# Performance work log

Measured on AMD Instinct MI355X. Metric: run time of the kernel, lower is better.

The kernel has to match this reference:

```python
import jax, jax.numpy as jnp
import numpy as np

DIM = 1024
NUM_HEADS = 16
HEAD_DIM = DIM // NUM_HEADS
ROPE_THETA = 10000.0
SCALE = HEAD_DIM ** -0.5


def _apply_rope(x, cos, sin):
    # x: [B, H, S, head_dim]; cos/sin: [S, head_dim//2] (broadcast over B, H)
    x_even = x[..., 0::2]
    x_odd = x[..., 1::2]
    rot_even = x_even * cos - x_odd * sin
    rot_odd = x_even * sin + x_odd * cos
    # interleave back: stack on last axis then flatten, matching torch .stack(-1).flatten(-2)
    return jnp.stack([rot_even, rot_odd], axis=-1).reshape(x.shape)


def setup_inputs() -> dict:
    key = jax.random.key(0)
    k0, k1, k2 = jax.random.split(key, 3)
    B, S = 2, 2048
    x = jax.random.normal(k0, (B, S, DIM), dtype=jnp.float32)
    # small_init: std = sqrt(2 / (5*dim))
    qkv_w = jax.random.normal(k1, (3 * DIM, DIM), dtype=jnp.float32) * (2.0 / (5 * DIM)) ** 0.5
    qkv_b = jnp.zeros((3 * DIM,), dtype=jnp.float32)
    # wang_init: std = 2 / num_blocks / sqrt(dim) scaled
    out_w = jax.random.normal(k2, (DIM, DIM), dtype=jnp.float32) * (2.0 / DIM) ** 0.5 / 2.0
    out_b = jnp.zeros((DIM,), dtype=jnp.float32)
    return {"x": x, "qkv_w": qkv_w, "qkv_b": qkv_b, "out_w": out_w, "out_b": out_b, "window_size": 512}


def reference(x, qkv_w, qkv_b, out_w, out_b, window_size):
    B, S, D = x.shape
    qkv = x @ qkv_w.T + qkv_b                          # [B, S, 3D]
    qkv = qkv.reshape(B, S, 3, NUM_HEADS, HEAD_DIM).transpose(2, 0, 3, 1, 4)
    q, k, v = qkv[0], qkv[1], qkv[2]                   # each [B, H, S, hd]

    pos = jnp.arange(S, dtype=jnp.float32)
    inv_freq = 1.0 / (ROPE_THETA ** (jnp.arange(0, HEAD_DIM, 2, dtype=jnp.float32) / HEAD_DIM))
    freqs = pos[:, None] * inv_freq                    # [S, hd//2]
    cos, sin = jnp.cos(freqs), jnp.sin(freqs)
    q = _apply_rope(q, cos, sin)
    k = _apply_rope(k, cos, sin)

    scores = jnp.einsum('bhqd,bhkd->bhqk', q, k) * SCALE
    i = jnp.arange(S)
    mask = (i[:, None] >= i[None, :]) & ((i[:, None] - i[None, :]) < window_size)  # causal sliding window
    scores = jnp.where(mask, scores, -jnp.inf)
    attn = jax.nn.softmax(scores, axis=-1)
    out = jnp.einsum('bhqk,bhkd->bhqd', attn, v)       # [B, H, S, hd]
    out = out.transpose(0, 2, 1, 3).reshape(B, S, D)
    return out @ out_w.T + out_b
```

## Files before the change

### kernel.cpp

```cpp
#include <hip/hip_runtime.h>
#include <hip/hip_bf16.h>
#include <cstdint>
#include <cstddef>

using bf16x8 = __attribute__((ext_vector_type(8))) short;
using f32x4  = __attribute__((ext_vector_type(4))) float;

#define MFMA16(a, b, c) __builtin_amdgcn_mfma_f32_16x16x32_bf16((a), (b), (c), 0, 0, 0)

__device__ __forceinline__ unsigned short f2bf(float f) {
    unsigned int u = __float_as_uint(f);
    u += 0x7fffu + ((u >> 16) & 1u);
    return (unsigned short)(u >> 16);
}
__device__ __forceinline__ uint32_t pack2bf(float a, float b) {
    __hip_bfloat162 h = __float22bfloat162_rn(float2{a, b});
    return *(uint32_t*)&h;
}
__device__ __forceinline__ float bf2f(short x) {
    return __uint_as_float(((uint32_t)(unsigned short)x) << 16);
}

__device__ __forceinline__ void gload_lds16(const void* g, void* l) {
    __builtin_amdgcn_global_load_lds(
        (const __attribute__((address_space(1))) void*)g,
        (__attribute__((address_space(3))) void*)l, 16, 0, 0);
}

#define S_LEN 2048
#define NHEAD 16
#define HDIM  64
#define DIM   1024
#define WIN   512
#define MROWS 4096

__global__ void prep(float* __restrict__ cosT, float* __restrict__ sinT,
                     const float* __restrict__ x, unsigned short* __restrict__ xb,
                     const float* __restrict__ qw, unsigned short* __restrict__ qwb,
                     const float* __restrict__ ow, unsigned short* __restrict__ owb) {
    int t = blockIdx.x * 256 + threadIdx.x;
    if (t < 65536) {
        int s = t >> 5, f = t & 31;
        float invf = powf(10000.0f, -(float)f / 32.0f);
        float ang = (float)s * invf;
        cosT[t] = cosf(ang);
        sinT[t] = sinf(ang);
        return;
    }
    int u = t - 65536;
    const float* src;
    unsigned short* dst;
    int i;
    if (u < 1048576)        { src = x;  dst = xb;  i = u * 4; }
    else if (u < 1835008)   { src = qw; dst = qwb; i = (u - 1048576) * 4; }
    else                    { src = ow; dst = owb; i = (u - 1835008) * 4; }
    float4 v = *(const float4*)(src + i);
    ushort4 o;
    o.x = f2bf(v.x); o.y = f2bf(v.y); o.z = f2bf(v.z); o.w = f2bf(v.w);
    *(ushort4*)(dst + i) = o;
}

__global__ __launch_bounds__(256) void gemm_qkv_fused(
        const unsigned short* __restrict__ A,
        const unsigned short* __restrict__ Bw,
        const float* __restrict__ bias,
        const float* __restrict__ cosT, const float* __restrict__ sinT,
        unsigned short* __restrict__ qbuf,
        unsigned short* __restrict__ kbuf,
        unsigned short* __restrict__ vtb) {
    __shared__ __align__(16) char smem_raw[34816];
    const int tid = threadIdx.x;
    const int lane = tid & 63, w = tid >> 6;
    const int wr = w >> 1, wc = w & 1, lm = lane & 15, lg = lane >> 4;
    const int bx = blockIdx.x, by = blockIdx.y;
    const int row0 = by * 128, col0 = bx * 128;
    const int plane = bx >> 3;
    const int h0 = (bx & 7) * 2;
    const int b = by >> 4, s_base = (by & 15) * 128;

    f32x4 acc[4][4];
#pragma unroll
    for (int m = 0; m < 4; ++m)
#pragma unroll
        for (int n = 0; n < 4; ++n) acc[m][n] = (f32x4){0.f, 0.f, 0.f, 0.f};

    short* As = (short*)smem_raw;
    short* Bs = (short*)(smem_raw + 16384);

    for (int kt = 0; kt < 16; ++kt) {
#pragma unroll
        for (int i = 0; i < 4; ++i) {
            int c = tid + 256 * i;
            int r = c >> 3, gs = (c & 7) ^ (r & 7);
            gload_lds16((const char*)A  + (size_t)(row0 + r) * 2048 + (size_t)kt * 128 + gs * 16, As + c * 8);
            gload_lds16((const char*)Bw + (size_t)(col0 + r) * 2048 + (size_t)kt * 128 + gs * 16, Bs + c * 8);
        }
        __syncthreads();
        bf16x8 af0[4], af1[4], bf0[4], bf1[4];
#pragma unroll
        for (int m = 0; m < 4; ++m) {
            int rl = wr * 64 + m * 16 + lm, rb = rl & 7;
            af0[m] = *(const bf16x8*)&As[rl * 64 + ((lg ^ rb) << 3)];
            af1[m] = *(const bf16x8*)&As[rl * 64 + (((lg + 4) ^ rb) << 3)];
        }
#pragma unroll
        for (int n = 0; n < 4; ++n) {
            int rl = wc * 64 + n * 16 + lm, rb = rl & 7;
            bf0[n] = *(const bf16x8*)&Bs[rl * 64 + ((lg ^ rb) << 3)];
            bf1[n] = *(const bf16x8*)&Bs[rl * 64 + (((lg + 4) ^ rb) << 3)];
        }
#pragma unroll
        for (int m = 0; m < 4; ++m)
#pragma unroll
            for (int n = 0; n < 4; ++n) {
                acc[m][n] = MFMA16(af0[m], bf0[n], acc[m][n]);
                acc[m][n] = MFMA16(af1[m], bf1[n], acc[m][n]);
            }
        __syncthreads();
    }

    unsigned short (*tile)[136] = (unsigned short(*)[136])smem_raw;
    const int lane8 = tid & 7, idx = tid >> 3;

    if (plane < 2) {
#pragma unroll
        for (int m = 0; m < 4; ++m)
#pragma unroll
            for (int n = 0; n < 4; ++n) {
                int colL = wc * 64 + n * 16 + lm;
                float bv = bias[col0 + colL];
#pragma unroll
                for (int r = 0; r < 4; ++r)
                    tile[wr * 64 + m * 16 + lg * 4 + r][colL] = f2bf(acc[m][n][r] + bv);
            }
    } else {
#pragma unroll
        for (int m = 0; m < 4; ++m)
#pragma unroll
            for (int n = 0; n < 4; ++n) {
                int colL = wc * 64 + n * 16 + lm;
                float bv = bias[col0 + colL];
                uint2 pk;
                pk.x = pack2bf(acc[m][n][0] + bv, acc[m][n][1] + bv);
                pk.y = pack2bf(acc[m][n][2] + bv, acc[m][n][3] + bv);
                *(uint2*)&tile[colL][wr * 64 + m * 16 + lg * 4] = pk;
            }
    }
    __syncthreads();

    if (plane < 2) {
        unsigned short* dstp = (plane == 0) ? qbuf : kbuf;
        const float qsc = (plane == 0) ? 0.125f : 1.0f;
        int d0 = lane8 * 8;
#pragma unroll
        for (int j = 0; j < 4; ++j) {
            int srow = idx + 32 * j;
            int s = s_base + srow;
            float4 c4 = *(const float4*)&cosT[s * 32 + (d0 >> 1)];
            float4 s4 = *(const float4*)&sinT[s * 32 + (d0 >> 1)];
#pragma unroll
            for (int hh = 0; hh < 2; ++hh) {
                bf16x8 v = *(const bf16x8*)&tile[srow][hh * 64 + d0];
                float e0 = bf2f(v[0]), o0 = bf2f(v[1]);
                float e1 = bf2f(v[2]), o1 = bf2f(v[3]);
                float e2 = bf2f(v[4]), o2 = bf2f(v[5]);
                float e3 = bf2f(v[6]), o3 = bf2f(v[7]);
                uint4 pk;
                pk.x = pack2bf((e0 * c4.x - o0 * s4.x) * qsc, (e0 * s4.x + o0 * c4.x) * qsc);
                pk.y = pack2bf((e1 * c4.y - o1 * s4.y) * qsc, (e1 * s4.y + o1 * c4.y) * qsc);
                pk.z = pack2bf((e2 * c4.z - o2 * s4.z) * qsc, (e2 * s4.z + o2 * c4.z) * qsc);
                pk.w = pack2bf((e3 * c4.w - o3 * s4.w) * qsc, (e3 * s4.w + o3 * c4.w) * qsc);
                int h = h0 + hh;
                *(uint4*)&dstp[(((size_t)(b * NHEAD + h)) * S_LEN + s) * 64 + d0] = pk;
            }
        }
    } else {
#pragma unroll
        for (int rr = 0; rr < 4; ++rr) {
            int hd = rr * 32 + idx;
            int hh = hd >> 6, d = hd & 63, h = h0 + hh;
#pragma unroll
            for (int j = 0; j < 2; ++j) {
                int s0 = lane8 * 8 + j * 64;
                bf16x8 v = *(const bf16x8*)&tile[hd][s0];
                *(bf16x8*)&vtb[((size_t)(b * NHEAD + h) * 64 + d) * S_LEN +
                               s_base + s0] = v;
            }
        }
    }
}

__global__ __launch_bounds__(256) void gemm_out(const unsigned short* __restrict__ A,
                                                const unsigned short* __restrict__ Bw,
                                                const float* __restrict__ bias,
                                                float* __restrict__ Cout) {
    __shared__ __align__(16) char smem_raw[24576];
    const int tid = threadIdx.x;
    const int lane = tid & 63, w = tid >> 6;
    const int wr = w >> 1, wc = w & 1, lm = lane & 15, lg = lane >> 4;
    const int row0 = blockIdx.y * 128, col0 = blockIdx.x * 64;

    f32x4 acc[4][2];
#pragma unroll
    for (int m = 0; m < 4; ++m)
#pragma unroll
        for (int n = 0; n < 2; ++n) acc[m][n] = (f32x4){0.f, 0.f, 0.f, 0.f};

    short* As = (short*)smem_raw;
    short* Bs = (short*)(smem_raw + 16384);

    for (int kt = 0; kt < 16; ++kt) {
#pragma unroll
        for (int i = 0; i < 4; ++i) {
            int c = tid + 256 * i;
            int r = c >> 3, gs = (c & 7) ^ (r & 7);
            gload_lds16((const char*)A + (size_t)(row0 + r) * 2048 + (size_t)kt * 128 + gs * 16, As + c * 8);
        }
#pragma unroll
        for (int i = 0; i < 2; ++i) {
            int c = tid + 256 * i;
            int r = c >> 3, gs = (c & 7) ^ (r & 7);
            gload_lds16((const char*)Bw + (size_t)(col0 + r) * 2048 + (size_t)kt * 128 + gs * 16, Bs + c * 8);
        }
        __syncthreads();
        bf16x8 af0[4], af1[4], bf0[2], bf1[2];
#pragma unroll
        for (int m = 0; m < 4; ++m) {
            int rl = wr * 64 + m * 16 + lm, rb = rl & 7;
            af0[m] = *(const bf16x8*)&As[rl * 64 + ((lg ^ rb) << 3)];
            af1[m] = *(const bf16x8*)&As[rl * 64 + (((lg + 4) ^ rb) << 3)];
        }
#pragma unroll
        for (int n = 0; n < 2; ++n) {
            int rl = wc * 32 + n * 16 + lm, rb = rl & 7;
            bf0[n] = *(const bf16x8*)&Bs[rl * 64 + ((lg ^ rb) << 3)];
            bf1[n] = *(const bf16x8*)&Bs[rl * 64 + (((lg + 4) ^ rb) << 3)];
        }
#pragma unroll
        for (int m = 0; m < 4; ++m)
#pragma unroll
            for (int n = 0; n < 2; ++n) {
                acc[m][n] = MFMA16(af0[m], bf0[n], acc[m][n]);
                acc[m][n] = MFMA16(af1[m], bf1[n], acc[m][n]);
            }
        __syncthreads();
    }

#pragma unroll
    for (int m = 0; m < 4; ++m) {
        int row = row0 + wr * 64 + m * 16 + lg * 4;
#pragma unroll
        for (int n = 0; n < 2; ++n) {
            int col = col0 + wc * 32 + n * 16 + lm;
            float bv = bias[col];
#pragma unroll
            for (int r = 0; r < 4; ++r)
                Cout[(size_t)(row + r) * DIM + col] = acc[m][n][r] + bv;
        }
    }
}

__global__ __launch_bounds__(256) void attn(const unsigned short* __restrict__ qb,
                                            const unsigned short* __restrict__ kb,
                                            const unsigned short* __restrict__ vt,
                                            unsigned short* __restrict__ ao) {
    const int p = blockIdx.x;
    const int L = (p & 7) * 128 + (p >> 3);
    const int qblk = L & 31, bh = L >> 5;
    const int b = bh >> 4, h = bh & 15;
    const int tid = threadIdx.x, w = tid >> 6, lane = tid & 63;
    const int lm = lane & 15, lg = lane >> 4;
    const unsigned short* Qb = qb + (size_t)bh * S_LEN * 64;
    const unsigned short* Kb = kb + (size_t)bh * S_LEN * 64;
    const unsigned short* Vt = vt + (size_t)bh * 64 * S_LEN;
    const int q0 = qblk * 64 + w * 16;

    __shared__ short Ks[128 * 64];
    __shared__ short Vs[64 * 128];
    __shared__ short Plds[4][16 * 64];
    short* Pw = Plds[w];

    bf16x8 aq0 = *(const bf16x8*)&Qb[(q0 + lm) * 64 + lg * 8];
    bf16x8 aq1 = *(const bf16x8*)&Qb[(q0 + lm) * 64 + lg * 8 + 32];

    f32x4 o[4];
#pragma unroll
    for (int n = 0; n < 4; ++n) o[n] = (f32x4){0.f, 0.f, 0.f, 0.f};
    float lsum = 0.f;

    const int qq = q0 + lm;
    const int t0_64 = qblk >= 8 ? qblk - 8 : 0;
    const int first = t0_64 >> 1, last = qblk >> 1;
    const int sw = lm & 7;

    for (int kt = first; kt <= last; ++kt) {
#pragma unroll
        for (int i = 0; i < 4; ++i) {
            int c = tid + 256 * i;
            int r = c >> 3, g = (c & 7) ^ (r & 7);
            gload_lds16(Kb + (size_t)(kt * 128 + r) * 64 + g * 8, &Ks[c * 8]);
        }
#pragma unroll
        for (int i = 0; i < 4; ++i) {
            int c = tid + 256 * i;
            int r = c >> 4, g = (c & 15) ^ (r & 7);
            gload_lds16(Vt + (size_t)r * S_LEN + kt * 128 + g * 8, &Vs[c * 8]);
        }
        __syncthreads();
#pragma unroll
        for (int half = 0; half < 2; ++half) {
            const int h64 = kt * 2 + half;
            if (h64 < t0_64 || h64 > qblk) continue;
            const int kbase = h64 * 64;
            f32x4 sT[4];
            __builtin_amdgcn_s_setprio(1);
#pragma unroll
            for (int n = 0; n < 4; ++n) {
                int rl = half * 64 + n * 16 + lm;
                bf16x8 bk0 = *(const bf16x8*)&Ks[rl * 64 + ((lg ^ sw) << 3)];
                bf16x8 bk1 = *(const bf16x8*)&Ks[rl * 64 + (((lg + 4) ^ sw) << 3)];
                f32x4 z = (f32x4){0.f, 0.f, 0.f, 0.f};
                z = MFMA16(bk0, aq0, z);
                sT[n] = MFMA16(bk1, aq1, z);
            }
            __builtin_amdgcn_s_setprio(0);
#pragma unroll
            for (int n = 0; n < 4; ++n) {
                int kk0 = kbase + n * 16 + lg * 4;
#pragma unroll
                for (int r = 0; r < 4; ++r) {
                    int d = qq - (kk0 + r);
                    float pv = ((unsigned)d < (unsigned)WIN) ? __expf(sT[n][r]) : 0.f;
                    sT[n][r] = pv;
                    lsum += pv;
                }
                uint2 pk;
                pk.x = pack2bf(sT[n][0], sT[n][1]);
                pk.y = pack2bf(sT[n][2], sT[n][3]);
                *(uint2*)&Pw[lm * 64 + ((((2 * n + (lg >> 1)) ^ sw) << 3) + ((lg & 1) << 2))] = pk;
            }
            bf16x8 ap0 = *(const bf16x8*)&Pw[lm * 64 + ((lg ^ sw) << 3)];
            bf16x8 ap1 = *(const bf16x8*)&Pw[lm * 64 + (((lg + 4) ^ sw) << 3)];
            __builtin_amdgcn_s_setprio(1);
#pragma unroll
            for (int n = 0; n < 4; ++n) {
                int rl = n * 16 + lm;
                bf16x8 bv0 = *(const bf16x8*)&Vs[rl * 128 + half * 64 + ((lg ^ sw) << 3)];
                bf16x8 bv1 = *(const bf16x8*)&Vs[rl * 128 + half * 64 + (((lg + 4) ^ sw) << 3)];
                o[n] = MFMA16(ap0, bv0, o[n]);
                o[n] = MFMA16(ap1, bv1, o[n]);
            }
            __builtin_amdgcn_s_setprio(0);
        }
        __syncthreads();
    }
    lsum += __shfl_xor(lsum, 16, 64);
    lsum += __shfl_xor(lsum, 32, 64);
    float linv = 1.f / lsum;
    float lrow[4];
#pragma unroll
    for (int r = 0; r < 4; ++r) lrow[r] = __shfl(linv, lg * 4 + r, 64);
#pragma unroll
    for (int n = 0; n < 4; ++n)
#pragma unroll
        for (int r = 0; r < 4; ++r) {
            int row = b * S_LEN + q0 + lg * 4 + r;
            int col = h * 64 + n * 16 + lm;
            ao[(size_t)row * DIM + col] = f2bf(o[n][r] * lrow[r]);
        }
}

extern "C" void kernel_launch(void* const* d_in, const int* in_sizes, int n_in,
                              void* d_out, int out_size, void* d_ws, size_t ws_size,
                              hipStream_t stream) {
    const float* x      = (const float*)d_in[0];
    const float* qkv_w  = (const float*)d_in[1];
    const float* qkv_b  = (const float*)d_in[2];
    const float* out_w  = (const float*)d_in[3];
    const float* out_b  = (const float*)d_in[4];
    (void)in_sizes; (void)n_in; (void)out_size; (void)ws_size;

    char* ws = (char*)d_ws;
    float*          cosT = (float*)(ws + 0);
    float*          sinT = (float*)(ws + 262144);
    unsigned short* xb   = (unsigned short*)(ws + 524288);
    unsigned short* wqb  = (unsigned short*)(ws + 8912896);
    unsigned short* owb  = (unsigned short*)(ws + 15204352);
    unsigned short* qbuf = (unsigned short*)(ws + 17301504);
    unsigned short* kbuf = (unsigned short*)(ws + 25690112);
    unsigned short* vtb  = (unsigned short*)(ws + 34078720);
    unsigned short* aob  = (unsigned short*)(ws + 42467328);

    prep<<<8448, 256, 0, stream>>>(cosT, sinT, x, xb, qkv_w, wqb, out_w, owb);

    gemm_qkv_fused<<<dim3(24, 32), 256, 0, stream>>>(xb, wqb, qkv_b, cosT, sinT,
                                                     qbuf, kbuf, vtb);

    attn<<<1024, 256, 0, stream>>>(qbuf, kbuf, vtb, aob);

    gemm_out<<<dim3(16, 32), 256, 0, stream>>>(aob, owb, out_b, (float*)d_out);
}
```

Baseline: 96.12 us.

## Rewrite QKV GEMM as 256x256 tile with double-buffered async LDS pipeline

The fused QKV GEMM+RoPE kernel moves from 128x128 tiles with 4 waves to 256x256 tiles with 8 waves, 128 KB of LDS and double-buffered A/B stages. Global loads into LDS are issued while MFMAs run, using vmcnt waits, raw barriers and s_setprio. The goal is to hide load latency and raise data reuse per tile. In exchange the grid shrinks to 192 blocks, fewer than the 256 CUs, and the epilogue is split into two passes that reuse the staging LDS.

```diff
diff --git a/kernel.cpp b/kernel.cpp
--- a/kernel.cpp
+++ b/kernel.cpp
@@ -60,7 +60,7 @@
     *(ushort4*)(dst + i) = o;
 }
 
-__global__ __launch_bounds__(256) void gemm_qkv_fused(
+__global__ __launch_bounds__(512, 2) void gemm_qkv8(
         const unsigned short* __restrict__ A,
         const unsigned short* __restrict__ Bw,
         const float* __restrict__ bias,
@@ -68,124 +68,207 @@
         unsigned short* __restrict__ qbuf,
         unsigned short* __restrict__ kbuf,
         unsigned short* __restrict__ vtb) {
-    __shared__ __align__(16) char smem_raw[34816];
+    __shared__ __align__(16) char smem[131072];
     const int tid = threadIdx.x;
     const int lane = tid & 63, w = tid >> 6;
-    const int wr = w >> 1, wc = w & 1, lm = lane & 15, lg = lane >> 4;
+    const int wr = w >> 2, wn = w & 3;
+    const int lm = lane & 15, lg = lane >> 4;
     const int bx = blockIdx.x, by = blockIdx.y;
-    const int row0 = by * 128, col0 = bx * 128;
-    const int plane = bx >> 3;
-    const int h0 = (bx & 7) * 2;
-    const int b = by >> 4, s_base = (by & 15) * 128;
-
-    f32x4 acc[4][4];
-#pragma unroll
-    for (int m = 0; m < 4; ++m)
-#pragma unroll
-        for (int n = 0; n < 4; ++n) acc[m][n] = (f32x4){0.f, 0.f, 0.f, 0.f};
-
-    short* As = (short*)smem_raw;
-    short* Bs = (short*)(smem_raw + 16384);
-
-    for (int kt = 0; kt < 16; ++kt) {
-#pragma unroll
-        for (int i = 0; i < 4; ++i) {
-            int c = tid + 256 * i;
-            int r = c >> 3, gs = (c & 7) ^ (r & 7);
-            gload_lds16((const char*)A  + (size_t)(row0 + r) * 2048 + (size_t)kt * 128 + gs * 16, As + c * 8);
-            gload_lds16((const char*)Bw + (size_t)(col0 + r) * 2048 + (size_t)kt * 128 + gs * 16, Bs + c * 8);
-        }
-        __syncthreads();
-        bf16x8 af0[4], af1[4], bf0[4], bf1[4];
-#pragma unroll
-        for (int m = 0; m < 4; ++m) {
-            int rl = wr * 64 + m * 16 + lm, rb = rl & 7;
-            af0[m] = *(const bf16x8*)&As[rl * 64 + ((lg ^ rb) << 3)];
-            af1[m] = *(const bf16x8*)&As[rl * 64 + (((lg + 4) ^ rb) << 3)];
-        }
-#pragma unroll
-        for (int n = 0; n < 4; ++n) {
-            int rl = wc * 64 + n * 16 + lm, rb = rl & 7;
-            bf0[n] = *(const bf16x8*)&Bs[rl * 64 + ((lg ^ rb) << 3)];
-            bf1[n] = *(const bf16x8*)&Bs[rl * 64 + (((lg + 4) ^ rb) << 3)];
-        }
-#pragma unroll
-        for (int m = 0; m < 4; ++m)
-#pragma unroll
-            for (int n = 0; n < 4; ++n) {
-                acc[m][n] = MFMA16(af0[m], bf0[n], acc[m][n]);
-                acc[m][n] = MFMA16(af1[m], bf1[n], acc[m][n]);
-            }
-        __syncthreads();
-    }
-
-    unsigned short (*tile)[136] = (unsigned short(*)[136])smem_raw;
+    const int row0 = by * 256, col0 = bx * 256;
+
+    f32x4 acc[8][4];
+#pragma unroll
+    for (int mf = 0; mf < 8; ++mf)
+#pragma unroll
+        for (int nf = 0; nf < 4; ++nf) acc[mf][nf] = (f32x4){0.f, 0.f, 0.f, 0.f};
+
+    short* SA0 = (short*)smem;
+    short* SB0 = (short*)(smem + 32768);
+    short* SA1 = (short*)(smem + 65536);
+    short* SB1 = (short*)(smem + 98304);
+
+    auto stageA = [&](int t) {
+        int tt = t & 15;
+        short* dst = (tt & 1) ? SA1 : SA0;
+#pragma unroll
+        for (int j = 0; j < 4; ++j) {
+            int slot = tid + 512 * j;
+            int r = slot >> 3, gp = slot & 7, gs = gp ^ (r & 7);
+            gload_lds16((const char*)A + (size_t)(row0 + r) * 2048 + tt * 128 + gs * 16,
+                        dst + slot * 8);
+        }
+    };
+    auto stageB = [&](int t) {
+        int tt = t & 15;
+        short* dst = (tt & 1) ? SB1 : SB0;
+#pragma unroll
+        for (int j = 0; j < 4; ++j) {
+            int slot = tid + 512 * j;
+            int r = slot >> 3, gp = slot & 7, gs = gp ^ (r & 7);
+            gload_lds16((const char*)Bw + (size_t)(col0 + r) * 2048 + tt * 128 + gs * 16,
+                        dst + slot * 8);
+        }
+    };
+
+    stageA(0); stageB(0); stageB(1);
+
+    const int rA = wr * 128;
+    const int rB = wn * 64;
+
+    for (int i = 0; i < 8; ++i) {
+        const int u = 2 * i, v = 2 * i + 1;
+        bf16x8 a[8], bq[4][2];
+        asm volatile("s_waitcnt vmcnt(4)" ::: "memory");
+        __builtin_amdgcn_s_barrier();
+#pragma unroll
+        for (int mf = 0; mf < 8; ++mf) {
+            int r = rA + mf * 16 + lm;
+            a[mf] = *(const bf16x8*)&SA0[r * 64 + ((lg ^ (r & 7)) << 3)];
+        }
+#pragma unroll
+        for (int nf = 0; nf < 4; ++nf) {
+            int r = rB + nf * 16 + lm;
+            bq[nf][0] = *(const bf16x8*)&SB0[r * 64 + ((lg ^ (r & 7)) << 3)];
+            bq[nf][1] = *(const bf16x8*)&SB0[r * 64 + (((lg + 4) ^ (r & 7)) << 3)];
+        }
+        stageA(v);
+        __builtin_amdgcn_s_setprio(1);
+#pragma unroll
+        for (int mf = 0; mf < 8; ++mf)
+#pragma unroll
+            for (int nf = 0; nf < 4; ++nf)
+                acc[mf][nf] = MFMA16(a[mf], bq[nf][0], acc[mf][nf]);
+        __builtin_amdgcn_s_setprio(0);
+        __builtin_amdgcn_s_barrier();
+#pragma unroll
+        for (int mf = 0; mf < 8; ++mf) {
+            int r = rA + mf * 16 + lm;
+            a[mf] = *(const bf16x8*)&SA0[r * 64 + (((lg + 4) ^ (r & 7)) << 3)];
+        }
+        stageB(u + 2);
+        __builtin_amdgcn_s_setprio(1);
+#pragma unroll
+        for (int mf = 0; mf < 8; ++mf)
+#pragma unroll
+            for (int nf = 0; nf < 4; ++nf)
+                acc[mf][nf] = MFMA16(a[mf], bq[nf][1], acc[mf][nf]);
+        __builtin_amdgcn_s_setprio(0);
+        asm volatile("s_waitcnt vmcnt(4)" ::: "memory");
+        __builtin_amdgcn_s_barrier();
+#pragma unroll
+        for (int mf = 0; mf < 8; ++mf) {
+            int r = rA + mf * 16 + lm;
+            a[mf] = *(const bf16x8*)&SA1[r * 64 + ((lg ^ (r & 7)) << 3)];
+        }
+#pragma unroll
+        for (int nf = 0; nf < 4; ++nf) {
+            int r = rB + nf * 16 + lm;
+            bq[nf][0] = *(const bf16x8*)&SB1[r * 64 + ((lg ^ (r & 7)) << 3)];
+            bq[nf][1] = *(const bf16x8*)&SB1[r * 64 + (((lg + 4) ^ (r & 7)) << 3)];
+        }
+        stageA(u + 2);
+        __builtin_amdgcn_s_setprio(1);
+#pragma unroll
+        for (int mf = 0; mf < 8; ++mf)
+#pragma unroll
+            for (int nf = 0; nf < 4; ++nf)
+                acc[mf][nf] = MFMA16(a[mf], bq[nf][0], acc[mf][nf]);
+        __builtin_amdgcn_s_setprio(0);
+        __builtin_amdgcn_s_barrier();
+#pragma unroll
+        for (int mf = 0; mf < 8; ++mf) {
+            int r = rA + mf * 16 + lm;
+            a[mf] = *(const bf16x8*)&SA1[r * 64 + (((lg + 4) ^ (r & 7)) << 3)];
+        }
+        stageB(v + 2);
+        __builtin_amdgcn_s_setprio(1);
+#pragma unroll
+        for (int mf = 0; mf < 8; ++mf)
+#pragma unroll
+            for (int nf = 0; nf < 4; ++nf)
+                acc[mf][nf] = MFMA16(a[mf], bq[nf][1], acc[mf][nf]);
+        __builtin_amdgcn_s_setprio(0);
+    }
+    asm volatile("s_waitcnt vmcnt(0)" ::: "memory");
+    __builtin_amdgcn_s_barrier();
+
+    const int plane = bx >> 2;
+    const int h0 = (bx & 3) * 4;
+    const int b = by >> 3, s_base = (by & 7) * 256;
     const int lane8 = tid & 7, idx = tid >> 3;
 
-    if (plane < 2) {
-#pragma unroll
-        for (int m = 0; m < 4; ++m)
-#pragma unroll
-            for (int n = 0; n < 4; ++n) {
-                int colL = wc * 64 + n * 16 + lm;
-                float bv = bias[col0 + colL];
-#pragma unroll
-                for (int r = 0; r < 4; ++r)
-                    tile[wr * 64 + m * 16 + lg * 4 + r][colL] = f2bf(acc[m][n][r] + bv);
-            }
-    } else {
-#pragma unroll
-        for (int m = 0; m < 4; ++m)
-#pragma unroll
-            for (int n = 0; n < 4; ++n) {
-                int colL = wc * 64 + n * 16 + lm;
-                float bv = bias[col0 + colL];
-                uint2 pk;
-                pk.x = pack2bf(acc[m][n][0] + bv, acc[m][n][1] + bv);
-                pk.y = pack2bf(acc[m][n][2] + bv, acc[m][n][3] + bv);
-                *(uint2*)&tile[colL][wr * 64 + m * 16 + lg * 4] = pk;
-            }
-    }
-    __syncthreads();
-
-    if (plane < 2) {
-        unsigned short* dstp = (plane == 0) ? qbuf : kbuf;
-        const float qsc = (plane == 0) ? 0.125f : 1.0f;
-        int d0 = lane8 * 8;
-#pragma unroll
-        for (int j = 0; j < 4; ++j) {
-            int srow = idx + 32 * j;
-            int s = s_base + srow;
-            float4 c4 = *(const float4*)&cosT[s * 32 + (d0 >> 1)];
-            float4 s4 = *(const float4*)&sinT[s * 32 + (d0 >> 1)];
-#pragma unroll
-            for (int hh = 0; hh < 2; ++hh) {
-                bf16x8 v = *(const bf16x8*)&tile[srow][hh * 64 + d0];
-                float e0 = bf2f(v[0]), o0 = bf2f(v[1]);
-                float e1 = bf2f(v[2]), o1 = bf2f(v[3]);
-                float e2 = bf2f(v[4]), o2 = bf2f(v[5]);
-                float e3 = bf2f(v[6]), o3 = bf2f(v[7]);
-                uint4 pk;
-                pk.x = pack2bf((e0 * c4.x - o0 * s4.x) * qsc, (e0 * s4.x + o0 * c4.x) * qsc);
-                pk.y = pack2bf((e1 * c4.y - o1 * s4.y) * qsc, (e1 * s4.y + o1 * c4.y) * qsc);
-                pk.z = pack2bf((e2 * c4.z - o2 * s4.z) * qsc, (e2 * s4.z + o2 * c4.z) * qsc);
-                pk.w = pack2bf((e3 * c4.w - o3 * s4.w) * qsc, (e3 * s4.w + o3 * c4.w) * qsc);
-                int h = h0 + hh;
-                *(uint4*)&dstp[(((size_t)(b * NHEAD + h)) * S_LEN + s) * 64 + d0] = pk;
-            }
-        }
-    } else {
-#pragma unroll
-        for (int rr = 0; rr < 4; ++rr) {
-            int hd = rr * 32 + idx;
-            int hh = hd >> 6, d = hd & 63, h = h0 + hh;
+#pragma unroll 1
+    for (int p = 0; p < 2; ++p) {
+        if (plane < 2) {
+            unsigned short (*tile)[264] = (unsigned short(*)[264])smem;
+            if (wr == p) {
+#pragma unroll
+                for (int mf = 0; mf < 8; ++mf)
+#pragma unroll
+                    for (int nf = 0; nf < 4; ++nf) {
+                        int colL = wn * 64 + nf * 16 + lm;
+                        float bv = bias[col0 + colL];
+#pragma unroll
+                        for (int r = 0; r < 4; ++r)
+                            tile[mf * 16 + lg * 4 + r][colL] = f2bf(acc[mf][nf][r] + bv);
+                    }
+            }
+            __syncthreads();
+            unsigned short* dstp = (plane == 0) ? qbuf : kbuf;
+            const float qsc = (plane == 0) ? 0.125f : 1.0f;
+            int d0 = lane8 * 8;
 #pragma unroll
             for (int j = 0; j < 2; ++j) {
-                int s0 = lane8 * 8 + j * 64;
-                bf16x8 v = *(const bf16x8*)&tile[hd][s0];
-                *(bf16x8*)&vtb[((size_t)(b * NHEAD + h) * 64 + d) * S_LEN +
-                               s_base + s0] = v;
-            }
+                int rloc = idx + 64 * j;
+                int s = s_base + p * 128 + rloc;
+                float4 c4 = *(const float4*)&cosT[s * 32 + (d0 >> 1)];
+                float4 s4 = *(const float4*)&sinT[s * 32 + (d0 >> 1)];
+#pragma unroll
+                for (int hh = 0; hh < 4; ++hh) {
+                    bf16x8 vld = *(const bf16x8*)&tile[rloc][hh * 64 + d0];
+                    float e0 = bf2f(vld[0]), o0 = bf2f(vld[1]);
+                    float e1 = bf2f(vld[2]), o1 = bf2f(vld[3]);
+                    float e2 = bf2f(vld[4]), o2 = bf2f(vld[5]);
+                    float e3 = bf2f(vld[6]), o3 = bf2f(vld[7]);
+                    uint4 pk;
+                    pk.x = pack2bf((e0 * c4.x - o0 * s4.x) * qsc, (e0 * s4.x + o0 * c4.x) * qsc);
+                    pk.y = pack2bf((e1 * c4.y - o1 * s4.y) * qsc, (e1 * s4.y + o1 * c4.y) * qsc);
+                    pk.z = pack2bf((e2 * c4.z - o2 * s4.z) * qsc, (e2 * s4.z + o2 * c4.z) * qsc);
+                    pk.w = pack2bf((e3 * c4.w - o3 * s4.w) * qsc, (e3 * s4.w + o3 * c4.w) * qsc);
+                    int h = h0 + hh;
+                    *(uint4*)&dstp[(((size_t)(b * NHEAD + h)) * S_LEN + s) * 64 + d0] = pk;
+                }
+            }
+            __syncthreads();
+        } else {
+            unsigned short (*tileT)[136] = (unsigned short(*)[136])smem;
+            if (wr == p) {
+#pragma unroll
+                for (int mf = 0; mf < 8; ++mf)
+#pragma unroll
+                    for (int nf = 0; nf < 4; ++nf) {
+                        int colL = wn * 64 + nf * 16 + lm;
+                        float bv = bias[col0 + colL];
+                        uint2 pk;
+                        pk.x = pack2bf(acc[mf][nf][0] + bv, acc[mf][nf][1] + bv);
+                        pk.y = pack2bf(acc[mf][nf][2] + bv, acc[mf][nf][3] + bv);
+                        *(uint2*)&tileT[colL][mf * 16 + lg * 4] = pk;
+                    }
+            }
+            __syncthreads();
+#pragma unroll
+            for (int ff = 0; ff < 4; ++ff) {
+                int f = ff * 64 + idx;
+                int hh = f >> 6, d = f & 63, h = h0 + hh;
+#pragma unroll
+                for (int j = 0; j < 2; ++j) {
+                    int s0 = lane8 * 8 + j * 64;
+                    bf16x8 vld = *(const bf16x8*)&tileT[f][s0];
+                    *(bf16x8*)&vtb[((size_t)(b * NHEAD + h) * 64 + d) * S_LEN +
+                                   s_base + p * 128 + s0] = vld;
+                }
+            }
+            __syncthreads();
         }
     }
 }
@@ -393,8 +476,8 @@
 
     prep<<<8448, 256, 0, stream>>>(cosT, sinT, x, xb, qkv_w, wqb, out_w, owb);
 
-    gemm_qkv_fused<<<dim3(24, 32), 256, 0, stream>>>(xb, wqb, qkv_b, cosT, sinT,
-                                                     qbuf, kbuf, vtb);
+    gemm_qkv8<<<dim3(12, 16), 512, 0, stream>>>(xb, wqb, qkv_b, cosT, sinT,
+                                                qbuf, kbuf, vtb);
 
     attn<<<1024, 256, 0, stream>>>(qbuf, kbuf, vtb, aob);
 
```

New measurement: 93.16 us, median of 2. -3.1%, faster.
